# Kernel optimization log

Hardware: AMD Instinct MI355X
Metric: run time of the kernel (lower is better)

The kernel has to match this reference:

```python
import jax, jax.numpy as jnp
import numpy as np

INF = 100000000.0
NUM_CLASSES = 80
RADIUS = 1.5

_SHAPES = [(100, 152), (50, 76), (25, 38), (13, 19), (7, 10)]
_STRIDES = [8, 16, 32, 64, 128]
_SOI = [(-1.0, 64.0), (64.0, 128.0), (128.0, 256.0), (256.0, 512.0), (512.0, INF)]


def _build_locations():
    locs, strs, sizes = [], [], []
    for (h, w), s, (lo, hi) in zip(_SHAPES, _STRIDES, _SOI):
        sx = np.arange(0, w * s, s, dtype=np.float32)
        sy = np.arange(0, h * s, s, dtype=np.float32)
        yy, xx = np.meshgrid(sy, sx, indexing='ij')
        l = np.stack([xx.ravel(), yy.ravel()], axis=1) + s // 2
        locs.append(l)
        strs.append(np.full(h * w, s, dtype=np.float32))
        sizes.append(np.tile(np.array([lo, hi], np.float32), (h * w, 1)))
    return (np.concatenate(locs, 0), np.concatenate(strs, 0), np.concatenate(sizes, 0))


def setup_inputs() -> dict:
    key = jax.random.key(0)
    locs, str_per, soi = _build_locations()  # K=20267
    B, G = 8, 64
    k1, k2, k3, k4 = jax.random.split(key, 4)
    cx = jax.random.uniform(k1, (B, G), minval=50.0, maxval=1150.0)
    cy = jax.random.uniform(k2, (B, G), minval=50.0, maxval=750.0)
    wh = jax.random.uniform(k3, (B, G, 2), minval=16.0, maxval=400.0)
    gt_boxes = jnp.stack([cx - wh[..., 0] / 2, cy - wh[..., 1] / 2,
                          cx + wh[..., 0] / 2, cy + wh[..., 1] / 2], axis=-1)
    gt_classes = jax.random.randint(k4, (B, G), 0, NUM_CLASSES)
    locations = jnp.asarray(locs)
    strides_per_loc = jnp.asarray(str_per)
    sizes_of_interest = jnp.asarray(soi)
    # FCOS-style single anchor per location: box centered at location, side = 4*stride
    anchors = jnp.concatenate([locations - 2.0 * strides_per_loc[:, None],
                               locations + 2.0 * strides_per_loc[:, None]], axis=-1)
    return {"locations": locations, "strides_per_loc": strides_per_loc,
            "sizes_of_interest": sizes_of_interest, "anchors": anchors,
            "gt_boxes": gt_boxes, "gt_classes": gt_classes}


def reference(locations, strides_per_loc, sizes_of_interest, anchors, gt_boxes, gt_classes):
    xs, ys = locations[:, 0], locations[:, 1]  # [K]

    def per_image(boxes, classes):
        # boxes [G,4], classes [G]
        l = xs[:, None] - boxes[None, :, 0]
        t = ys[:, None] - boxes[None, :, 1]
        r = boxes[None, :, 2] - xs[:, None]
        b = boxes[None, :, 3] - ys[:, None]
        reg = jnp.stack([l, t, r, b], axis=2)  # [K,G,4]
        # center sampling (get_sample_region), vectorized over per-location stride
        ccx = (boxes[:, 0] + boxes[:, 2]) / 2
        ccy = (boxes[:, 1] + boxes[:, 3]) / 2
        rad = (strides_per_loc * RADIUS)[:, None]  # [K,1]
        xmin = jnp.maximum(ccx[None, :] - rad, boxes[None, :, 0])
        ymin = jnp.maximum(ccy[None, :] - rad, boxes[None, :, 1])
        xmax = jnp.minimum(ccx[None, :] + rad, boxes[None, :, 2])
        ymax = jnp.minimum(ccy[None, :] + rad, boxes[None, :, 3])
        cb_min = jnp.minimum(jnp.minimum(xs[:, None] - xmin, ys[:, None] - ymin),
                             jnp.minimum(xmax - xs[:, None], ymax - ys[:, None]))
        in_box = cb_min > 0  # [K,G]
        max_reg = reg.max(axis=2)  # [K,G]
        cared = (max_reg >= sizes_of_interest[:, 0:1]) & (max_reg <= sizes_of_interest[:, 1:2])
        area = (boxes[:, 2] - boxes[:, 0]) * (boxes[:, 3] - boxes[:, 1])  # [G]
        loc2area = jnp.where(in_box & cared, area[None, :], INF)  # masked-fill with INF
        min_area = loc2area.min(axis=1)
        inds = jnp.argmin(loc2area, axis=1)  # [K], first min like torch
        cls = jnp.where(min_area == INF, NUM_CLASSES, classes[inds])
        reg_t = jnp.take_along_axis(reg, inds[:, None, None], axis=1)[:, 0, :]  # [K,4]
        matched = boxes[inds]  # [K,4]
        # Box2BoxTransform.get_deltas with unit weights
        aw = anchors[:, 2] - anchors[:, 0]
        ah = anchors[:, 3] - anchors[:, 1]
        acx = anchors[:, 0] + 0.5 * aw
        acy = anchors[:, 1] + 0.5 * ah
        gw = matched[:, 2] - matched[:, 0]
        gh = matched[:, 3] - matched[:, 1]
        gcx = matched[:, 0] + 0.5 * gw
        gcy = matched[:, 1] + 0.5 * gh
        deltas = jnp.stack([(gcx - acx) / aw, (gcy - acy) / ah,
                            jnp.log(gw / aw), jnp.log(gh / ah)], axis=1)  # [K,4]
        return cls, reg_t, deltas

    gt_cls, reg_targets, gt_deltas = jax.vmap(per_image)(gt_boxes, gt_classes)
    return gt_cls, reg_targets, gt_deltas
```

## Files before the change

### kernel.cpp

```cpp
#include <hip/hip_runtime.h>

#define NGT 64
#define NUM_CLASSES_F 80.0f
#define INF_F 100000000.0f
#define RADIUS_F 1.5f

__global__ __launch_bounds__(256, 8) void fcos_match_kernel(
    const float* __restrict__ locations,
    const float* __restrict__ strides_per_loc,
    const float* __restrict__ soi,
    const float* __restrict__ anchors,
    const float* __restrict__ gt_boxes,
    const int*   __restrict__ gt_classes,
    float* __restrict__ out,
    int L, int B)
{
    const int b = blockIdx.y;

    __shared__ float4 sbox[NGT];
    __shared__ float  sclsf[NGT];
    if (threadIdx.x < NGT) {
        const int j = threadIdx.x;
        sbox[j]  = reinterpret_cast<const float4*>(gt_boxes)[b * NGT + j];
        sclsf[j] = (float)gt_classes[b * NGT + j];
    }
    __syncthreads();

    const int  k      = threadIdx.x & 3;
    const int  p      = blockIdx.x * 64 + (threadIdx.x >> 2);
    const bool active = p < L;
    const int  i      = active ? p : 0;

    const float2 xy   = reinterpret_cast<const float2*>(locations)[i];
    const float  x    = xy.x, y = xy.y;
    const float  rad  = strides_per_loc[i] * RADIUS_F;
    const float2 lohi = reinterpret_cast<const float2*>(soi)[i];

    float minv = INF_F;
    int   ind  = k;

    #pragma unroll
    for (int s = 0; s < 16; ++s) {
        const int jg = (s << 2) | k;
        const float4 bx = sbox[jg];

        const float l = x - bx.x, t = y - bx.y;
        const float r = bx.z - x, d = bx.w - y;
        const float mx = fmaxf(fmaxf(fmaxf(l, t), r), d);
        const float mn = fminf(fminf(fminf(l, t), r), d);

        const float ccx = (bx.x + bx.z) * 0.5f;
        const float ccy = (bx.y + bx.w) * 0.5f;
        const float cx  = rad - fabsf(x - ccx);
        const float cy  = rad - fabsf(y - ccy);
        const float cmin = fminf(fminf(mn, cx), cy);

        const float g    = fminf(mx - lohi.x, lohi.y - mx);
        const float area = (bx.z - bx.x) * (bx.w - bx.y);
        const float v = ((cmin > 0.0f) && (g >= 0.0f)) ? area : INF_F;
        if (v < minv) { minv = v; ind = jg; }
    }

    {
        float vp = __shfl_xor(minv, 1);
        int   ip = __shfl_xor(ind, 1);
        if (vp < minv || (vp == minv && ip < ind)) { minv = vp; ind = ip; }
        vp = __shfl_xor(minv, 2);
        ip = __shfl_xor(ind, 2);
        if (vp < minv || (vp == minv && ip < ind)) { minv = vp; ind = ip; }
    }

    if (!active) return;

    const float4 mb = sbox[ind];
    const size_t o4 = (size_t)b * L + i;

    if (k == 0) {
        out[o4] = (minv == INF_F) ? NUM_CLASSES_F : sclsf[ind];
        float4* reg4 = reinterpret_cast<float4*>(out + (size_t)B * L) + o4;
        *reg4 = make_float4(x - mb.x, y - mb.y, mb.z - x, mb.w - y);
    } else if (k == 1) {
        const float4 an = reinterpret_cast<const float4*>(anchors)[i];
        const float aw  = an.z - an.x;
        const float ah  = an.w - an.y;
        const float acx = an.x + 0.5f * aw;
        const float acy = an.y + 0.5f * ah;
        const float gw  = mb.z - mb.x;
        const float gh  = mb.w - mb.y;
        const float gcx = mb.x + 0.5f * gw;
        const float gcy = mb.y + 0.5f * gh;

        float4* del4 = reinterpret_cast<float4*>(out + (size_t)B * L * 5) + o4;
        *del4 = make_float4((gcx - acx) / aw, (gcy - acy) / ah,
                            logf(gw / aw), logf(gh / ah));
    }
}

extern "C" void kernel_launch(void* const* d_in, const int* in_sizes, int n_in,
                              void* d_out, int out_size, void* d_ws, size_t ws_size,
                              hipStream_t stream) {
    const float* locations = (const float*)d_in[0];
    const float* strides   = (const float*)d_in[1];
    const float* soi       = (const float*)d_in[2];
    const float* anchors   = (const float*)d_in[3];
    const float* gt_boxes  = (const float*)d_in[4];
    const int*   gt_cls    = (const int*)d_in[5];
    float* out = (float*)d_out;

    const int L = in_sizes[1];
    const int B = in_sizes[5] / NGT;

    dim3 grid((L + 63) / 64, B);
    fcos_match_kernel<<<grid, dim3(256), 0, stream>>>(locations, strides, soi, anchors,
                                                      gt_boxes, gt_cls, out, L, B);
}
```

Baseline: 15.25 us.

## Precompute GT rank by area so per-location argmin becomes integer min

```diff
diff --git a/kernel.cpp b/kernel.cpp
--- a/kernel.cpp
+++ b/kernel.cpp
@@ -15,19 +15,47 @@
     float* __restrict__ out,
     int L, int B)
 {
-    const int b = blockIdx.y;
+    const int b   = blockIdx.y;
+    const int tid = threadIdx.x;
 
     __shared__ float4 sbox[NGT];
-    __shared__ float  sclsf[NGT];
-    if (threadIdx.x < NGT) {
-        const int j = threadIdx.x;
-        sbox[j]  = reinterpret_cast<const float4*>(gt_boxes)[b * NGT + j];
-        sclsf[j] = (float)gt_classes[b * NGT + j];
+    __shared__ float4 sbd[NGT];
+    __shared__ float  sarea[NGT];
+    __shared__ int    sinv[NGT];
+
+    if (tid < NGT) {
+        const float4 bx = reinterpret_cast<const float4*>(gt_boxes)[b * NGT + tid];
+        sbox[tid]  = bx;
+        sarea[tid] = (bx.z - bx.x) * (bx.w - bx.y);
+        sbd[tid]   = make_float4((bx.x + bx.z) * 0.5f,
+                                 (bx.y + bx.w) * 0.5f,
+                                 0.0f,
+                                 (float)gt_classes[b * NGT + tid]);
     }
     __syncthreads();
 
-    const int  k      = threadIdx.x & 3;
-    const int  p      = blockIdx.x * 64 + (threadIdx.x >> 2);
+    {
+        const int j  = tid >> 2;
+        const int kk = tid & 3;
+        const float aj = sarea[j];
+        int cnt = 0;
+        #pragma unroll
+        for (int it = 0; it < 16; ++it) {
+            const int kb = (kk << 4) + it;
+            const float ak = sarea[kb];
+            cnt += ((ak < aj) || (ak == aj && kb < j)) ? 1 : 0;
+        }
+        cnt += __shfl_xor(cnt, 1);
+        cnt += __shfl_xor(cnt, 2);
+        if (kk == 0) {
+            reinterpret_cast<float*>(&sbd[j])[2] = __uint_as_float((unsigned)cnt);
+            sinv[cnt] = j;
+        }
+    }
+    __syncthreads();
+
+    const int  k      = tid & 3;
+    const int  p      = blockIdx.x * 64 + (tid >> 2);
     const bool active = p < L;
     const int  i      = active ? p : 0;
 
@@ -36,47 +64,42 @@
     const float  rad  = strides_per_loc[i] * RADIUS_F;
     const float2 lohi = reinterpret_cast<const float2*>(soi)[i];
 
-    float minv = INF_F;
-    int   ind  = k;
+    unsigned mnr = 0xFFu;
 
     #pragma unroll
     for (int s = 0; s < 16; ++s) {
         const int jg = (s << 2) | k;
         const float4 bx = sbox[jg];
+        const float4 bd = sbd[jg];
 
         const float l = x - bx.x, t = y - bx.y;
         const float r = bx.z - x, d = bx.w - y;
         const float mx = fmaxf(fmaxf(fmaxf(l, t), r), d);
         const float mn = fminf(fminf(fminf(l, t), r), d);
 
-        const float ccx = (bx.x + bx.z) * 0.5f;
-        const float ccy = (bx.y + bx.w) * 0.5f;
-        const float cx  = rad - fabsf(x - ccx);
-        const float cy  = rad - fabsf(y - ccy);
+        const float cx = rad - fabsf(x - bd.x);
+        const float cy = rad - fabsf(y - bd.y);
         const float cmin = fminf(fminf(mn, cx), cy);
 
-        const float g    = fminf(mx - lohi.x, lohi.y - mx);
-        const float area = (bx.z - bx.x) * (bx.w - bx.y);
-        const float v = ((cmin > 0.0f) && (g >= 0.0f)) ? area : INF_F;
-        if (v < minv) { minv = v; ind = jg; }
+        const float g = fminf(mx - lohi.x, lohi.y - mx);
+        const bool valid = (cmin > 0.0f) && (g >= 0.0f);
+
+        const unsigned rk = valid ? __float_as_uint(bd.z) : 0xFFu;
+        mnr = min(mnr, rk);
     }
 
-    {
-        float vp = __shfl_xor(minv, 1);
-        int   ip = __shfl_xor(ind, 1);
-        if (vp < minv || (vp == minv && ip < ind)) { minv = vp; ind = ip; }
-        vp = __shfl_xor(minv, 2);
-        ip = __shfl_xor(ind, 2);
-        if (vp < minv || (vp == minv && ip < ind)) { minv = vp; ind = ip; }
-    }
+    mnr = min(mnr, (unsigned)__shfl_xor((int)mnr, 1));
+    mnr = min(mnr, (unsigned)__shfl_xor((int)mnr, 2));
 
     if (!active) return;
 
+    const bool none = (mnr == 0xFFu);
+    const int  ind  = none ? 0 : sinv[mnr];
     const float4 mb = sbox[ind];
     const size_t o4 = (size_t)b * L + i;
 
     if (k == 0) {
-        out[o4] = (minv == INF_F) ? NUM_CLASSES_F : sclsf[ind];
+        out[o4] = none ? NUM_CLASSES_F : sbd[ind].w;
         float4* reg4 = reinterpret_cast<float4*>(out + (size_t)B * L) + o4;
         *reg4 = make_float4(x - mb.x, y - mb.y, mb.z - x, mb.w - y);
     } else if (k == 1) {
```

After: 14.09 us. -7.6%, faster.
